# Kernel tuning notes

Measured on AMD Instinct MI355X. Metric: run time of the kernel, lower is better.

## Reference

```python
import jax, jax.numpy as jnp
import numpy as np

N, INP, H, FH = 768, 256, 4, 64  # nodes, inp_dim, heads, hidden-per-head (out_dim=H*FH=256)


def setup_inputs() -> dict:
    key = jax.random.key(0)
    k1, k2, k3, k4 = jax.random.split(key, 4)
    x = jax.random.normal(k1, (N, INP), dtype=jnp.float32)
    adj_mat = jax.random.randint(k2, (N, N, 1), 0, 2, dtype=jnp.int32)
    # nn.Linear weights: W.weight [H*FH, INP], a.weight [1, FH] (stored as [FH])
    W = jax.random.uniform(k3, (H * FH, INP), dtype=jnp.float32, minval=-0.1, maxval=0.1)
    a = jax.random.uniform(k4, (FH,), dtype=jnp.float32, minval=-0.1, maxval=0.1)
    return {"x": x, "adj_mat": adj_mat, "W": W, "a": a}


def reference(x, adj_mat, W, a):
    n = x.shape[0]
    Wx = (x @ W.T).reshape(n, H, FH)                       # [N,H,F]
    # dense pairwise features: Wx_ij[i,j] = Wx[i] + Wx[j] (symmetric sum)
    s = Wx[:, None, :, :] + Wx[None, :, :, :]             # [N,N,H,F]
    # dynamic attention: a(leaky_relu(Wx_ij))
    e = jnp.einsum('ijhf,f->ijh', jax.nn.leaky_relu(s, 0.2), a)  # [N,N,H]
    e = jnp.where(adj_mat == 0, -jnp.inf, e)               # adj [N,N,1] broadcasts over H
    att = jax.nn.softmax(e, axis=1)                        # softmax over neighbors j
    # dropout is identity in eval/reference mode
    xh = jnp.einsum('ijh,jhf->ihf', att, Wx)               # [N,H,F]
    return xh.reshape(n, H * FH)                           # concat heads
```

## Files before the change

kernel.cpp:

```cpp
#include <hip/hip_runtime.h>
#include <hip/hip_bf16.h>

#define NN   768
#define INP  256
#define NH   4
#define FH   64
#define DOUT 256

typedef _Float16 h2 __attribute__((ext_vector_type(2)));
typedef _Float16 h8 __attribute__((ext_vector_type(8)));
typedef float    f4 __attribute__((ext_vector_type(4)));

union HU { unsigned int u; h2 h; };

__device__ __forceinline__ float b2f(unsigned short u) {
    union { unsigned int i; float f; } v;
    v.i = ((unsigned int)u) << 16;
    return v.f;
}
__device__ __forceinline__ unsigned short f2b(float f) {
    union { float f; unsigned int i; } v; v.f = f;
    unsigned int lsb = (v.i >> 16) & 1;
    v.i += 0x7FFFu + lsb;
    return (unsigned short)(v.i >> 16);
}

__device__ __forceinline__ unsigned int pkadd(unsigned int a, unsigned int b) {
    HU x, y, r; x.u = a; y.u = b; r.h = x.h + y.h; return r.u;
}
#if defined(__has_builtin)
#if __has_builtin(__builtin_amdgcn_fdot2)
#define HAVE_FDOT2 1
#endif
#endif
__device__ __forceinline__ float dot2abs(unsigned int a, unsigned int s, float acc) {
    HU x, y; x.u = a; y.u = s & 0x7FFF7FFFu;
#ifdef HAVE_FDOT2
    return __builtin_amdgcn_fdot2(x.h, y.h, acc, false);
#else
    return acc + (float)x.h.x * (float)y.h.x + (float)x.h.y * (float)y.h.y;
#endif
}

__device__ __forceinline__ int detect_bf16(const void* xin) {
    const unsigned int* xw = (const unsigned int*)xin;
    unsigned int u = xw[(threadIdx.x & 63) * 7];
    unsigned int e = (u >> 7) & 0xFFu;
    unsigned long long m = __ballot(e >= 124u && e <= 127u);
    return (__popcll(m) >= 32) ? 1 : 0;
}

__global__ __launch_bounds__(256) void wx_kernel(
    const void* __restrict__ xin, const void* __restrict__ Win,
    const void* __restrict__ ain,
    _Float16* __restrict__ Wxf, _Float16* __restrict__ BT,
    float* __restrict__ lin, unsigned int* __restrict__ apk,
    int* __restrict__ flagout)
{
    const int isbf = detect_bf16(xin);
    __shared__ float xs[4][INP];
    __shared__ float sa[64];
    const int tid = threadIdx.x;
    const int r0  = blockIdx.x * 4;

    if (isbf) {
        const unsigned short* xp = (const unsigned short*)xin + r0 * INP;
        for (int idx = tid; idx < 4 * INP; idx += 256)
            xs[idx >> 8][idx & 255] = b2f(xp[idx]);
    } else {
        const float* xp = (const float*)xin + r0 * INP;
        for (int idx = tid; idx < 4 * INP; idx += 256)
            xs[idx >> 8][idx & 255] = xp[idx];
    }
    if (tid < 64)
        sa[tid] = isbf ? b2f(((const unsigned short*)ain)[tid])
                       : ((const float*)ain)[tid];
    __syncthreads();

    const int o = tid;
    float acc0 = 0.f, acc1 = 0.f, acc2 = 0.f, acc3 = 0.f;
    if (isbf) {
        const unsigned short* wr = (const unsigned short*)Win + o * INP;
        #pragma unroll 4
        for (int k = 0; k < INP; k += 4) {
            ushort4 u = *(const ushort4*)(wr + k);
            float4 w = make_float4(b2f(u.x), b2f(u.y), b2f(u.z), b2f(u.w));
            float4 x0 = *(const float4*)&xs[0][k];
            float4 x1 = *(const float4*)&xs[1][k];
            float4 x2 = *(const float4*)&xs[2][k];
            float4 x3 = *(const float4*)&xs[3][k];
            acc0 += x0.x * w.x + x0.y * w.y + x0.z * w.z + x0.w * w.w;
            acc1 += x1.x * w.x + x1.y * w.y + x1.z * w.z + x1.w * w.w;
            acc2 += x2.x * w.x + x2.y * w.y + x2.z * w.z + x2.w * w.w;
            acc3 += x3.x * w.x + x3.y * w.y + x3.z * w.z + x3.w * w.w;
        }
    } else {
        const float* wr = (const float*)Win + o * INP;
        #pragma unroll 4
        for (int k = 0; k < INP; k += 4) {
            float4 w = *(const float4*)(wr + k);
            float4 x0 = *(const float4*)&xs[0][k];
            float4 x1 = *(const float4*)&xs[1][k];
            float4 x2 = *(const float4*)&xs[2][k];
            float4 x3 = *(const float4*)&xs[3][k];
            acc0 += x0.x * w.x + x0.y * w.y + x0.z * w.z + x0.w * w.w;
            acc1 += x1.x * w.x + x1.y * w.y + x1.z * w.z + x1.w * w.w;
            acc2 += x2.x * w.x + x2.y * w.y + x2.z * w.z + x2.w * w.w;
            acc3 += x3.x * w.x + x3.y * w.y + x3.z * w.z + x3.w * w.w;
        }
    }

    Wxf[(r0 + 0) * DOUT + o] = (_Float16)acc0;
    Wxf[(r0 + 1) * DOUT + o] = (_Float16)acc1;
    Wxf[(r0 + 2) * DOUT + o] = (_Float16)acc2;
    Wxf[(r0 + 3) * DOUT + o] = (_Float16)acc3;
    {
        HU u0, u1;
        u0.h = h2{(_Float16)acc0, (_Float16)acc1};
        u1.h = h2{(_Float16)acc2, (_Float16)acc3};
        uint2 pv; pv.x = u0.u; pv.y = u1.u;
        *(uint2*)(BT + (size_t)o * NN + r0) = pv;
    }

    const int f = tid & 63;
    const int h = tid >> 6;
    if (blockIdx.x == 0) {
        if (tid == 0) *flagout = isbf;
        if (tid < 32) {
            HU p; p.h = h2{(_Float16)(0.4f * sa[2 * tid]),
                           (_Float16)(0.4f * sa[2 * tid + 1])};
            apk[tid] = p.u;
        }
    }

    const float af = 0.6f * sa[f];
    float v0 = af * acc0, v1 = af * acc1, v2 = af * acc2, v3 = af * acc3;
    #pragma unroll
    for (int d = 1; d < 64; d <<= 1) {
        v0 += __shfl_xor(v0, d);
        v1 += __shfl_xor(v1, d);
        v2 += __shfl_xor(v2, d);
        v3 += __shfl_xor(v3, d);
    }
    if (f == 0) {
        lin[(r0 + 0) * NH + h] = v0;
        lin[(r0 + 1) * NH + h] = v1;
        lin[(r0 + 2) * NH + h] = v2;
        lin[(r0 + 3) * NH + h] = v3;
    }
}

#define EP 772
#define KP 776
__global__ __launch_bounds__(256) void gat_kernel(
    const _Float16* __restrict__ Wxf,
    const _Float16* __restrict__ BT,
    const float* __restrict__ lin,
    const unsigned int* __restrict__ apk,
    const int* __restrict__ adj,
    void* __restrict__ outv,
    const int* __restrict__ flag)
{
    __shared__ float E[16][EP];
    __shared__ __align__(16) _Float16 P[16][KP];
    __shared__ float S[16];

    const int b    = blockIdx.x;
    const int h    = b & 3, it = b >> 2;
    const int i0   = it * 16;
    const int tid  = threadIdx.x;
    const int wv   = tid >> 6;
    const int lane = tid & 63;

    uint4 ap[8];
    #pragma unroll
    for (int c = 0; c < 8; ++c) ap[c] = *(const uint4*)(apk + c * 4);

    for (int s = 0; s < 3; ++s) {
        const int j = wv * 192 + s * 64 + lane;
        uint4 wj[8];
        #pragma unroll
        for (int c = 0; c < 8; ++c)
            wj[c] = *(const uint4*)(Wxf + (size_t)j * DOUT + h * FH + c * 8);
        const float linj = lin[j * NH + h];

        for (int r = 0; r < 16; ++r) {
            const int i = i0 + r;
            const int adjv = adj[(size_t)i * NN + j];
            const float lini = lin[i * NH + h];
            float acc = 0.f;
            #pragma unroll
            for (int c = 0; c < 8; ++c) {
                const uint4 wiv = *(const uint4*)(Wxf + (size_t)i * DOUT + h * FH + c * 8);
                acc = dot2abs(ap[c].x, pkadd(wiv.x, wj[c].x), acc);
                acc = dot2abs(ap[c].y, pkadd(wiv.y, wj[c].y), acc);
                acc = dot2abs(ap[c].z, pkadd(wiv.z, wj[c].z), acc);
                acc = dot2abs(ap[c].w, pkadd(wiv.w, wj[c].w), acc);
            }
            E[r][j] = adjv ? (acc + lini + linj) : -__builtin_inff();
        }
    }
    __syncthreads();

    #pragma unroll
    for (int rr = 0; rr < 4; ++rr) {
        const int row = wv * 4 + rr;
        float v[12];
        float m = -__builtin_inff();
        #pragma unroll
        for (int c = 0; c < 12; ++c) {
            v[c] = E[row][c * 64 + lane];
            m = fmaxf(m, v[c]);
        }
        #pragma unroll
        for (int d = 1; d < 64; d <<= 1) m = fmaxf(m, __shfl_xor(m, d));
        if (m == -__builtin_inff()) m = 0.f;
        float sum = 0.f;
        #pragma unroll
        for (int c = 0; c < 12; ++c) {
            const float ev = __expf(v[c] - m);
            sum += ev;
            P[row][c * 64 + lane] = (_Float16)ev;
        }
        #pragma unroll
        for (int d = 1; d < 64; d <<= 1) sum += __shfl_xor(sum, d);
        if (lane == 0) S[row] = fmaxf(sum, 1e-30f);
    }
    __syncthreads();

    const int mrow = lane & 15;
    const int quad = lane >> 4;
    const int n0   = wv * 16;
    f4 acc = {0.f, 0.f, 0.f, 0.f};
    const _Float16* bbase = BT + ((size_t)(h * FH + n0 + mrow)) * NN + quad * 8;
    const _Float16* abase = &P[mrow][quad * 8];
    #pragma unroll 4
    for (int k0 = 0; k0 < NN; k0 += 32) {
        const h8 af = *(const h8*)(abase + k0);
        const h8 bf = *(const h8*)(bbase + k0);
        acc = __builtin_amdgcn_mfma_f32_16x16x32_f16(af, bf, acc, 0, 0, 0);
    }

    const int isbf = *flag;
    #pragma unroll
    for (int r = 0; r < 4; ++r) {
        const int row = quad * 4 + r;
        const float val = acc[r] / S[row];
        const size_t oidx = (size_t)(i0 + row) * DOUT + h * FH + n0 + mrow;
        if (isbf) ((unsigned short*)outv)[oidx] = f2b(val);
        else      ((float*)outv)[oidx] = val;
    }
}

extern "C" void kernel_launch(void* const* d_in, const int* in_sizes, int n_in,
                              void* d_out, int out_size, void* d_ws, size_t ws_size,
                              hipStream_t stream) {
    const void* px = d_in[0]; const void* padj = d_in[1];
    const void* pW = d_in[2]; const void* pa  = d_in[3];
    for (int t = 0; t < n_in; ++t) {
        switch (in_sizes[t]) {
            case NN * INP:   px   = d_in[t]; break;
            case NN * NN:    padj = d_in[t]; break;
            case DOUT * INP: pW   = d_in[t]; break;
            case FH:         pa   = d_in[t]; break;
        }
    }

    char* ws = (char*)d_ws;
    int*          flag = (int*)ws;
    unsigned int* apk  = (unsigned int*)(ws + 256);
    float*        lin  = (float*)(ws + 1024);
    _Float16*     Wxf  = (_Float16*)(ws + 16384);
    _Float16*     BT   = (_Float16*)(ws + 409600);

    wx_kernel<<<NN / 4, 256, 0, stream>>>(px, pW, pa, Wxf, BT, lin, apk, flag);
    gat_kernel<<<(NN / 16) * NH, 256, 0, stream>>>(Wxf, BT, lin, apk,
                                                   (const int*)padj, d_out, flag);
}
```

Measured before the change: 98.05 us.

## Split-K the projection kernel and shrink GAT row blocks to raise parallelism

The projection kernel now runs 1024 threads per block, splitting the K dimension four ways and reducing the partial sums through shared memory. The attention kernel processes 4 rows per block instead of 16, which gives 768 blocks instead of 192. Each block caches the Wx_i rows in LDS, uses four independent dot accumulators to break the dependency chain, and zero-pads the unused rows of the MFMA A tile. The aim is to fill more CUs, at the cost of recomputing Wx_j loads per block and wasting three quarters of the MFMA work.

```diff
diff --git a/kernel.cpp b/kernel.cpp
--- a/kernel.cpp
+++ b/kernel.cpp
@@ -50,7 +50,7 @@
     return (__popcll(m) >= 32) ? 1 : 0;
 }
 
-__global__ __launch_bounds__(256) void wx_kernel(
+__global__ __launch_bounds__(1024) void wx_kernel(
     const void* __restrict__ xin, const void* __restrict__ Win,
     const void* __restrict__ ain,
     _Float16* __restrict__ Wxf, _Float16* __restrict__ BT,
@@ -60,49 +60,50 @@
     const int isbf = detect_bf16(xin);
     __shared__ float xs[4][INP];
     __shared__ float sa[64];
+    __shared__ float part[3][4][256];
     const int tid = threadIdx.x;
     const int r0  = blockIdx.x * 4;
+    const int o   = tid & 255;
+    const int ks  = tid >> 8;
 
     if (isbf) {
         const unsigned short* xp = (const unsigned short*)xin + r0 * INP;
-        for (int idx = tid; idx < 4 * INP; idx += 256)
-            xs[idx >> 8][idx & 255] = b2f(xp[idx]);
+        xs[tid >> 8][tid & 255] = b2f(xp[tid]);
     } else {
         const float* xp = (const float*)xin + r0 * INP;
-        for (int idx = tid; idx < 4 * INP; idx += 256)
-            xs[idx >> 8][idx & 255] = xp[idx];
+        xs[tid >> 8][tid & 255] = xp[tid];
     }
     if (tid < 64)
         sa[tid] = isbf ? b2f(((const unsigned short*)ain)[tid])
                        : ((const float*)ain)[tid];
     __syncthreads();
 
-    const int o = tid;
+    const int k0 = ks * 64;
     float acc0 = 0.f, acc1 = 0.f, acc2 = 0.f, acc3 = 0.f;
     if (isbf) {
-        const unsigned short* wr = (const unsigned short*)Win + o * INP;
+        const unsigned short* wr = (const unsigned short*)Win + o * INP + k0;
         #pragma unroll 4
-        for (int k = 0; k < INP; k += 4) {
+        for (int k = 0; k < 64; k += 4) {
             ushort4 u = *(const ushort4*)(wr + k);
             float4 w = make_float4(b2f(u.x), b2f(u.y), b2f(u.z), b2f(u.w));
-            float4 x0 = *(const float4*)&xs[0][k];
-            float4 x1 = *(const float4*)&xs[1][k];
-            float4 x2 = *(const float4*)&xs[2][k];
-            float4 x3 = *(const float4*)&xs[3][k];
+            float4 x0 = *(const float4*)&xs[0][k0 + k];
+            float4 x1 = *(const float4*)&xs[1][k0 + k];
+            float4 x2 = *(const float4*)&xs[2][k0 + k];
+            float4 x3 = *(const float4*)&xs[3][k0 + k];
             acc0 += x0.x * w.x + x0.y * w.y + x0.z * w.z + x0.w * w.w;
             acc1 += x1.x * w.x + x1.y * w.y + x1.z * w.z + x1.w * w.w;
             acc2 += x2.x * w.x + x2.y * w.y + x2.z * w.z + x2.w * w.w;
             acc3 += x3.x * w.x + x3.y * w.y + x3.z * w.z + x3.w * w.w;
         }
     } else {
-        const float* wr = (const float*)Win + o * INP;
+        const float* wr = (const float*)Win + o * INP + k0;
         #pragma unroll 4
-        for (int k = 0; k < INP; k += 4) {
+        for (int k = 0; k < 64; k += 4) {
             float4 w = *(const float4*)(wr + k);
-            float4 x0 = *(const float4*)&xs[0][k];
-            float4 x1 = *(const float4*)&xs[1][k];
-            float4 x2 = *(const float4*)&xs[2][k];
-            float4 x3 = *(const float4*)&xs[3][k];
+            float4 x0 = *(const float4*)&xs[0][k0 + k];
+            float4 x1 = *(const float4*)&xs[1][k0 + k];
+            float4 x2 = *(const float4*)&xs[2][k0 + k];
+            float4 x3 = *(const float4*)&xs[3][k0 + k];
             acc0 += x0.x * w.x + x0.y * w.y + x0.z * w.z + x0.w * w.w;
             acc1 += x1.x * w.x + x1.y * w.y + x1.z * w.z + x1.w * w.w;
             acc2 += x2.x * w.x + x2.y * w.y + x2.z * w.z + x2.w * w.w;
@@ -110,49 +111,64 @@
         }
     }
 
-    Wxf[(r0 + 0) * DOUT + o] = (_Float16)acc0;
-    Wxf[(r0 + 1) * DOUT + o] = (_Float16)acc1;
-    Wxf[(r0 + 2) * DOUT + o] = (_Float16)acc2;
-    Wxf[(r0 + 3) * DOUT + o] = (_Float16)acc3;
-    {
-        HU u0, u1;
-        u0.h = h2{(_Float16)acc0, (_Float16)acc1};
-        u1.h = h2{(_Float16)acc2, (_Float16)acc3};
-        uint2 pv; pv.x = u0.u; pv.y = u1.u;
-        *(uint2*)(BT + (size_t)o * NN + r0) = pv;
-    }
-
-    const int f = tid & 63;
-    const int h = tid >> 6;
-    if (blockIdx.x == 0) {
-        if (tid == 0) *flagout = isbf;
-        if (tid < 32) {
-            HU p; p.h = h2{(_Float16)(0.4f * sa[2 * tid]),
-                           (_Float16)(0.4f * sa[2 * tid + 1])};
-            apk[tid] = p.u;
-        }
-    }
-
-    const float af = 0.6f * sa[f];
-    float v0 = af * acc0, v1 = af * acc1, v2 = af * acc2, v3 = af * acc3;
-    #pragma unroll
-    for (int d = 1; d < 64; d <<= 1) {
-        v0 += __shfl_xor(v0, d);
-        v1 += __shfl_xor(v1, d);
-        v2 += __shfl_xor(v2, d);
-        v3 += __shfl_xor(v3, d);
-    }
-    if (f == 0) {
-        lin[(r0 + 0) * NH + h] = v0;
-        lin[(r0 + 1) * NH + h] = v1;
-        lin[(r0 + 2) * NH + h] = v2;
-        lin[(r0 + 3) * NH + h] = v3;
-    }
-}
-
+    if (ks > 0) {
+        part[ks - 1][0][o] = acc0;
+        part[ks - 1][1][o] = acc1;
+        part[ks - 1][2][o] = acc2;
+        part[ks - 1][3][o] = acc3;
+    }
+    __syncthreads();
+    if (ks == 0) {
+        acc0 += part[0][0][o] + part[1][0][o] + part[2][0][o];
+        acc1 += part[0][1][o] + part[1][1][o] + part[2][1][o];
+        acc2 += part[0][2][o] + part[1][2][o] + part[2][2][o];
+        acc3 += part[0][3][o] + part[1][3][o] + part[2][3][o];
+
+        Wxf[(r0 + 0) * DOUT + o] = (_Float16)acc0;
+        Wxf[(r0 + 1) * DOUT + o] = (_Float16)acc1;
+        Wxf[(r0 + 2) * DOUT + o] = (_Float16)acc2;
+        Wxf[(r0 + 3) * DOUT + o] = (_Float16)acc3;
+        {
+            HU u0, u1;
+            u0.h = h2{(_Float16)acc0, (_Float16)acc1};
+            u1.h = h2{(_Float16)acc2, (_Float16)acc3};
+            uint2 pv; pv.x = u0.u; pv.y = u1.u;
+            *(uint2*)(BT + (size_t)o * NN + r0) = pv;
+        }
+
+        const int f = tid & 63;
+        const int h = tid >> 6;
+        if (blockIdx.x == 0) {
+            if (tid == 0) *flagout = isbf;
+            if (tid < 32) {
+                HU p; p.h = h2{(_Float16)(0.4f * sa[2 * tid]),
+                               (_Float16)(0.4f * sa[2 * tid + 1])};
+                apk[tid] = p.u;
+            }
+        }
+
+        const float af = 0.6f * sa[f];
+        float v0 = af * acc0, v1 = af * acc1, v2 = af * acc2, v3 = af * acc3;
+        #pragma unroll
+        for (int d = 1; d < 64; d <<= 1) {
+            v0 += __shfl_xor(v0, d);
+            v1 += __shfl_xor(v1, d);
+            v2 += __shfl_xor(v2, d);
+            v3 += __shfl_xor(v3, d);
+        }
+        if (f == 0) {
+            lin[(r0 + 0) * NH + h] = v0;
+            lin[(r0 + 1) * NH + h] = v1;
+            lin[(r0 + 2) * NH + h] = v2;
+            lin[(r0 + 3) * NH + h] = v3;
+        }
+    }
+}
+
+#define RB 4
 #define EP 772
 #define KP 776
-__global__ __launch_bounds__(256) void gat_kernel(
+__global__ __launch_bounds__(256, 3) void gat_kernel(
     const _Float16* __restrict__ Wxf,
     const _Float16* __restrict__ BT,
     const float* __restrict__ lin,
@@ -161,50 +177,67 @@
     void* __restrict__ outv,
     const int* __restrict__ flag)
 {
-    __shared__ float E[16][EP];
+    __shared__ float E[RB][EP];
     __shared__ __align__(16) _Float16 P[16][KP];
-    __shared__ float S[16];
+    __shared__ float S[RB];
+    __shared__ __align__(16) _Float16 WI[RB * FH];
 
     const int b    = blockIdx.x;
     const int h    = b & 3, it = b >> 2;
-    const int i0   = it * 16;
+    const int i0   = it * RB;
     const int tid  = threadIdx.x;
     const int wv   = tid >> 6;
     const int lane = tid & 63;
 
+    {
+        uint4 z = {0u, 0u, 0u, 0u};
+        uint4* pz = (uint4*)&P[RB][0];
+        #pragma unroll 2
+        for (int idx = tid; idx < ((16 - RB) * KP * 2) / 16; idx += 256)
+            pz[idx] = z;
+    }
+    if (tid < RB * FH / 2) {
+        ((unsigned int*)WI)[tid] =
+            *(const unsigned int*)(Wxf + (size_t)(i0 + (tid >> 5)) * DOUT
+                                   + h * FH + (tid & 31) * 2);
+    }
+
     uint4 ap[8];
     #pragma unroll
     for (int c = 0; c < 8; ++c) ap[c] = *(const uint4*)(apk + c * 4);
+    float lini[RB];
+    #pragma unroll
+    for (int r = 0; r < RB; ++r) lini[r] = lin[(i0 + r) * NH + h];
+    __syncthreads();
 
     for (int s = 0; s < 3; ++s) {
-        const int j = wv * 192 + s * 64 + lane;
+        const int j = s * 256 + tid;
         uint4 wj[8];
         #pragma unroll
         for (int c = 0; c < 8; ++c)
             wj[c] = *(const uint4*)(Wxf + (size_t)j * DOUT + h * FH + c * 8);
         const float linj = lin[j * NH + h];
 
-        for (int r = 0; r < 16; ++r) {
-            const int i = i0 + r;
-            const int adjv = adj[(size_t)i * NN + j];
-            const float lini = lin[i * NH + h];
-            float acc = 0.f;
+        #pragma unroll
+        for (int r = 0; r < RB; ++r) {
+            const int adjv = adj[(size_t)(i0 + r) * NN + j];
+            float a0 = 0.f, a1 = 0.f, a2 = 0.f, a3 = 0.f;
             #pragma unroll
             for (int c = 0; c < 8; ++c) {
-                const uint4 wiv = *(const uint4*)(Wxf + (size_t)i * DOUT + h * FH + c * 8);
-                acc = dot2abs(ap[c].x, pkadd(wiv.x, wj[c].x), acc);
-                acc = dot2abs(ap[c].y, pkadd(wiv.y, wj[c].y), acc);
-                acc = dot2abs(ap[c].z, pkadd(wiv.z, wj[c].z), acc);
-                acc = dot2abs(ap[c].w, pkadd(wiv.w, wj[c].w), acc);
+                const uint4 wiv = *(const uint4*)&WI[r * FH + c * 8];
+                a0 = dot2abs(ap[c].x, pkadd(wiv.x, wj[c].x), a0);
+                a1 = dot2abs(ap[c].y, pkadd(wiv.y, wj[c].y), a1);
+                a2 = dot2abs(ap[c].z, pkadd(wiv.z, wj[c].z), a2);
+                a3 = dot2abs(ap[c].w, pkadd(wiv.w, wj[c].w), a3);
             }
-            E[r][j] = adjv ? (acc + lini + linj) : -__builtin_inff();
-        }
-    }
-    __syncthreads();
-
-    #pragma unroll
-    for (int rr = 0; rr < 4; ++rr) {
-        const int row = wv * 4 + rr;
+            const float acc = (a0 + a1) + (a2 + a3);
+            E[r][j] = adjv ? (acc + lini[r] + linj) : -__builtin_inff();
+        }
+    }
+    __syncthreads();
+
+    {
+        const int row = wv;
         float v[12];
         float m = -__builtin_inff();
         #pragma unroll
@@ -242,13 +275,14 @@
     }
 
     const int isbf = *flag;
-    #pragma unroll
-    for (int r = 0; r < 4; ++r) {
-        const int row = quad * 4 + r;
-        const float val = acc[r] / S[row];
-        const size_t oidx = (size_t)(i0 + row) * DOUT + h * FH + n0 + mrow;
-        if (isbf) ((unsigned short*)outv)[oidx] = f2b(val);
-        else      ((float*)outv)[oidx] = val;
+    if (quad == 0) {
+        #pragma unroll
+        for (int r = 0; r < RB; ++r) {
+            const float val = acc[r] / S[r];
+            const size_t oidx = (size_t)(i0 + r) * DOUT + h * FH + n0 + mrow;
+            if (isbf) ((unsigned short*)outv)[oidx] = f2b(val);
+            else      ((float*)outv)[oidx] = val;
+        }
     }
 }
 
@@ -273,7 +307,7 @@
     _Float16*     Wxf  = (_Float16*)(ws + 16384);
     _Float16*     BT   = (_Float16*)(ws + 409600);
 
-    wx_kernel<<<NN / 4, 256, 0, stream>>>(px, pW, pa, Wxf, BT, lin, apk, flag);
-    gat_kernel<<<(NN / 16) * NH, 256, 0, stream>>>(Wxf, BT, lin, apk,
+    wx_kernel<<<NN / 4, 1024, 0, stream>>>(px, pW, pa, Wxf, BT, lin, apk, flag);
+    gat_kernel<<<(NN / RB) * NH, 256, 0, stream>>>(Wxf, BT, lin, apk,
                                                    (const int*)padj, d_out, flag);
 }
```

After: 100.0 us. 2.0% more time.
